# Performance work log

Hardware: AMD Instinct MI355X
Metric: run time of the kernel (lower is better)

The kernel has to match this reference:

```python
import jax, jax.numpy as jnp
import numpy as np

B, T, C, D = 8, 4096, 1024, 128  # batch, seq (=block_size), dim_embd, head_features

def setup_inputs() -> dict:
    key = jax.random.key(0)
    k1, k2, k3, k4 = jax.random.split(key, 4)
    s = 0.02
    return {
        "x": jax.random.normal(k1, (B, T, C), dtype=jnp.float32),
        "wq": jax.random.normal(k2, (C, D), dtype=jnp.float32) * s,
        "wk": jax.random.normal(k3, (C, D), dtype=jnp.float32) * s,
        "wv": jax.random.normal(k4, (C, D), dtype=jnp.float32) * s,
    }

def reference(x, wq, wk, wv):
    # q,k,v: [B,T,D]
    q = jnp.einsum('btc,cd->btd', x, wq)
    k = jnp.einsum('btc,cd->btd', x, wk)
    v = jnp.einsum('btc,cd->btd', x, wv)
    scale = k.shape[-1] ** -0.5
    wei = jnp.einsum('bqd,bkd->bqk', q, k) * scale  # [B,T,T]
    causal = jnp.tril(jnp.ones((T, T), dtype=bool))
    wei = jnp.where(causal, wei, -jnp.inf)
    attn = jax.nn.softmax(wei, axis=-1)  # dropout p=0.0 -> identity
    out = jnp.einsum('bqk,bkd->bqd', attn, v)  # [B,T,D]
    return out
```

## Files before the change

### kernel.cpp

```cpp
#include <hip/hip_runtime.h>

#define TT 4096
#define CC 1024
#define DD 128

typedef __attribute__((ext_vector_type(8))) short s16x8;
typedef __attribute__((ext_vector_type(4))) short s16x4;
typedef __attribute__((ext_vector_type(8))) __bf16 bf16x8;
typedef __attribute__((ext_vector_type(4))) float f32x4;

__device__ __forceinline__ short f2bf(float f) {
    union { float f; unsigned u; } v; v.f = f;
    unsigned r = v.u + 0x7fffu + ((v.u >> 16) & 1u);
    return (short)(r >> 16);
}

__device__ __forceinline__ unsigned cvt_pk(float lo, float hi) {
    unsigned r;
    asm("v_cvt_pk_bf16_f32 %0, %1, %2" : "=v"(r) : "v"(lo), "v"(hi));
    return r;
}

__device__ __forceinline__ f32x4 mfma16(s16x8 a, s16x8 b, f32x4 c) {
    return __builtin_amdgcn_mfma_f32_16x16x32_bf16(
        __builtin_bit_cast(bf16x8, a), __builtin_bit_cast(bf16x8, b), c, 0, 0, 0);
}

__device__ __forceinline__ void gload_lds16(const short* g, short* l) {
    __builtin_amdgcn_global_load_lds(
        (const __attribute__((address_space(1))) void*)g,
        (__attribute__((address_space(3))) void*)l, 16, 0, 0);
}

__global__ void wt_kernel(const float* __restrict__ wq, const float* __restrict__ wk,
                          const float* __restrict__ wv, short* __restrict__ wT) {
    int idx = blockIdx.x * 256 + threadIdx.x;
    int d = idx & 127;
    int c = (idx >> 7) & 1023;
    int wsel = idx >> 17;
    const float* w = (wsel == 0) ? wq : (wsel == 1) ? wk : wv;
    float v = w[(size_t)c * DD + d];
    if (wsel == 0) v *= 0.08838834764831845f;
    wT[(size_t)wsel * DD * CC + (size_t)d * CC + c] = f2bf(v);
}

__global__ __launch_bounds__(512)
void qkv_kernel(const float* __restrict__ x, const short* __restrict__ wT,
                short* __restrict__ qo, short* __restrict__ ko, short* __restrict__ vTo) {
    __shared__ short lw[2][384 * 64];
    const int mt = blockIdx.x;
    const int tid = threadIdx.x, lane = tid & 63, wid = tid >> 6;
    const int l15 = lane & 15, g = lane >> 4;
    const int wm = wid >> 1, wn = wid & 1;
    const int arow = mt * 128 + wm * 32 + l15;
    const float* xr0 = x + (size_t)arow * CC + g * 8;
    const float* xr1 = xr0 + (size_t)16 * CC;

    const f32x4 fz = {0.f, 0.f, 0.f, 0.f};
    f32x4 acc[2][12];
#pragma unroll
    for (int mr = 0; mr < 2; mr++)
#pragma unroll
        for (int nr = 0; nr < 12; nr++) acc[mr][nr] = fz;

    const int swr = wid * 48;
    const short* wsrc = wT + (size_t)(swr + (lane >> 3)) * CC + (lane & 7) * 8;

    float4 pa[2][2][2];
#define LOADA(kc) do { \
    _Pragma("unroll") for (int mr_ = 0; mr_ < 2; mr_++) \
    _Pragma("unroll") for (int ks_ = 0; ks_ < 2; ks_++) { \
        const float* p_ = (mr_ ? xr1 : xr0) + (kc) * 64 + ks_ * 32; \
        pa[mr_][ks_][0] = *(const float4*)p_; \
        pa[mr_][ks_][1] = *(const float4*)(p_ + 4); } \
} while (0)
#define STAGEW(kc, buf) do { \
    _Pragma("unroll") for (int j_ = 0; j_ < 6; j_++) \
        gload_lds16(wsrc + (size_t)(j_ * 8) * CC + (kc) * 64, &lw[buf][(swr + j_ * 8) * 64]); \
} while (0)

    LOADA(0);
    STAGEW(0, 0);
    asm volatile("s_waitcnt vmcnt(0)" ::: "memory");
    __builtin_amdgcn_s_barrier();
    int cur = 0;

    for (int kc = 0; kc < 16; kc++) {
        s16x8 af[2][2];
#pragma unroll
        for (int mr = 0; mr < 2; mr++)
#pragma unroll
            for (int ks = 0; ks < 2; ks++) {
                union { unsigned u[4]; s16x8 v; } cv;
                cv.u[0] = cvt_pk(pa[mr][ks][0].x, pa[mr][ks][0].y);
                cv.u[1] = cvt_pk(pa[mr][ks][0].z, pa[mr][ks][0].w);
                cv.u[2] = cvt_pk(pa[mr][ks][1].x, pa[mr][ks][1].y);
                cv.u[3] = cvt_pk(pa[mr][ks][1].z, pa[mr][ks][1].w);
                af[mr][ks] = cv.v;
            }
        if (kc < 15) { LOADA(kc + 1); STAGEW(kc + 1, cur ^ 1); }
        __builtin_amdgcn_s_setprio(1);
#pragma unroll
        for (int ks = 0; ks < 2; ks++)
#pragma unroll
            for (int nr = 0; nr < 12; nr++) {
                const s16x8 bfg = *(const s16x8*)
                    &lw[cur][(wn * 192 + nr * 16 + l15) * 64 + ks * 32 + g * 8];
                acc[0][nr] = mfma16(af[0][ks], bfg, acc[0][nr]);
                acc[1][nr] = mfma16(af[1][ks], bfg, acc[1][nr]);
            }
        __builtin_amdgcn_s_setprio(0);
        asm volatile("s_waitcnt vmcnt(0) lgkmcnt(0)" ::: "memory");
        __builtin_amdgcn_s_barrier();
        cur ^= 1;
    }

    const int bidx = mt >> 5;
    const int tb = (mt & 31) * 128 + wm * 32;
#pragma unroll
    for (int mr = 0; mr < 2; mr++)
#pragma unroll
        for (int nr = 0; nr < 12; nr++) {
            const int n = wn * 192 + nr * 16 + l15;
            if (n < 256) {
                short* dst; int d;
                if (n < 128) { dst = qo; d = n; } else { dst = ko; d = n - 128; }
#pragma unroll
                for (int i = 0; i < 4; i++) {
                    int t = tb + mr * 16 + g * 4 + i;
                    dst[((size_t)bidx * TT + t) * DD + d] = f2bf(acc[mr][nr][i]);
                }
            } else {
                const int d = n - 256;
                const int t = tb + mr * 16 + g * 4;
                uint2 u;
                u.x = cvt_pk(acc[mr][nr][0], acc[mr][nr][1]);
                u.y = cvt_pk(acc[mr][nr][2], acc[mr][nr][3]);
                *(uint2*)(vTo + ((size_t)bidx * DD + d) * TT + t) = u;
            }
        }
}

__device__ __forceinline__ void attn_stage(const short* kT, const short* vT, int kv0,
                                           short* lkb, short* lvb, int wid, int lane) {
#pragma unroll
    for (int j = 0; j < 4; j++) {
        int rbk = wid * 16 + j * 4;
        int rk = rbk + (lane >> 4);
        int ck = (lane & 15) ^ (rk & 7);
        gload_lds16(kT + (size_t)(kv0 + rk) * DD + ck * 8, lkb + rbk * 128);
        int rbv = wid * 32 + j * 8;
        int dv = rbv + (lane >> 3);
        int cv = (lane & 7) ^ (dv & 7);
        gload_lds16(vT + (size_t)dv * TT + kv0 + cv * 8, lvb + rbv * 64);
    }
}

__global__ __launch_bounds__(256)
void attn_kernel(const short* __restrict__ qb, const short* __restrict__ kb,
                 const short* __restrict__ vb, float* __restrict__ out) {
    __shared__ short lk[2][64 * 128];
    __shared__ short lv[2][128 * 64];
    __shared__ short lp[4 * 16 * 64];
    const int qt = 63 - blockIdx.x;
    const int b = blockIdx.y;
    const int tid = threadIdx.x, lane = tid & 63, wid = tid >> 6;
    const int l15 = lane & 15, g = lane >> 4;
    const int wq0 = qt * 64 + wid * 16;

    s16x8 qf[4];
    {
        const short* qp = qb + ((size_t)b * TT + wq0 + l15) * DD + g * 8;
#pragma unroll
        for (int ks = 0; ks < 4; ks++) qf[ks] = *(const s16x8*)(qp + ks * 32);
    }
    const f32x4 fz = {0.f, 0.f, 0.f, 0.f};
    f32x4 o[8];
#pragma unroll
    for (int n = 0; n < 8; n++) o[n] = fz;
    float rmax = -1e30f, rsum = 0.f;

    const short* kT = kb + (size_t)b * TT * DD;
    const short* vT = vb + (size_t)b * DD * TT;

    attn_stage(kT, vT, 0, lk[0], lv[0], wid, lane);
    asm volatile("s_waitcnt vmcnt(0)" ::: "memory");
    __builtin_amdgcn_s_barrier();
    int cur = 0;

    for (int kvt = 0; kvt <= qt; kvt++) {
        if (kvt < qt) attn_stage(kT, vT, (kvt + 1) * 64, lk[cur ^ 1], lv[cur ^ 1], wid, lane);
        const int kv0 = kvt * 64;
        const char* lkc = (const char*)&lk[cur][0];
        const char* lvc = (const char*)&lv[cur][0];

        f32x4 s[4];
        __builtin_amdgcn_s_setprio(1);
#pragma unroll
        for (int sub = 0; sub < 4; sub++) {
            f32x4 a = fz;
#pragma unroll
            for (int ks = 0; ks < 4; ks++) {
                int row = sub * 16 + l15;
                int byte = (row * 256 + ks * 64 + g * 16) ^ ((row & 7) << 4);
                s16x8 kf = *(const s16x8*)(lkc + byte);
                a = mfma16(kf, qf[ks], a);
            }
            s[sub] = a;
        }
        __builtin_amdgcn_s_setprio(0);
        if (kvt == qt) {
#pragma unroll
            for (int sub = 0; sub < 4; sub++)
#pragma unroll
                for (int i = 0; i < 4; i++) {
                    int k = kv0 + sub * 16 + 4 * g + i;
                    if (k > wq0 + l15) s[sub][i] = -1e30f;
                }
        }
        float m0 = s[0][0];
#pragma unroll
        for (int sub = 0; sub < 4; sub++)
#pragma unroll
            for (int i = 0; i < 4; i++) m0 = fmaxf(m0, s[sub][i]);
        m0 = fmaxf(m0, __shfl_xor(m0, 16));
        m0 = fmaxf(m0, __shfl_xor(m0, 32));
        float mnew = fmaxf(rmax, m0);
        float scal = __expf(rmax - mnew);
        rmax = mnew;
        float ls = 0.f;
#pragma unroll
        for (int sub = 0; sub < 4; sub++)
#pragma unroll
            for (int i = 0; i < 4; i++) {
                float p = __expf(s[sub][i] - mnew);
                s[sub][i] = p;
                ls += p;
            }
        ls += __shfl_xor(ls, 16);
        ls += __shfl_xor(ls, 32);
        rsum = rsum * scal + ls;
#pragma unroll
        for (int sub = 0; sub < 4; sub++) {
            uint2 w01;
            w01.x = cvt_pk(s[sub][0], s[sub][1]);
            w01.y = cvt_pk(s[sub][2], s[sub][3]);
            int byte = (l15 * 128 + sub * 32 + g * 8) ^ ((l15 & 7) << 4);
            *(uint2*)((char*)lp + wid * 2048 + byte) = w01;
        }
#pragma unroll
        for (int n = 0; n < 8; n++)
#pragma unroll
            for (int i = 0; i < 4; i++) o[n][i] *= scal;
        __builtin_amdgcn_s_setprio(1);
#pragma unroll
        for (int ks2 = 0; ks2 < 2; ks2++) {
            int pbyte = (l15 * 128 + ks2 * 64 + g * 16) ^ ((l15 & 7) << 4);
            s16x8 pf = *(const s16x8*)((const char*)lp + wid * 2048 + pbyte);
#pragma unroll
            for (int n = 0; n < 8; n++) {
                int vrow = n * 16 + l15;
                int vbyte = (vrow * 128 + ks2 * 64 + g * 16) ^ ((vrow & 7) << 4);
                s16x8 vf = *(const s16x8*)(lvc + vbyte);
                o[n] = mfma16(vf, pf, o[n]);
            }
        }
        __builtin_amdgcn_s_setprio(0);
        asm volatile("s_waitcnt vmcnt(0) lgkmcnt(0)" ::: "memory");
        __builtin_amdgcn_s_barrier();
        cur ^= 1;
    }
    float inv = 1.0f / rsum;
    float* orow = out + ((size_t)b * TT + wq0 + l15) * DD;
#pragma unroll
    for (int n = 0; n < 8; n++) {
        float4 r;
        r.x = o[n][0] * inv; r.y = o[n][1] * inv;
        r.z = o[n][2] * inv; r.w = o[n][3] * inv;
        *(float4*)(orow + n * 16 + 4 * g) = r;
    }
}

extern "C" void kernel_launch(void* const* d_in, const int* in_sizes, int n_in,
                              void* d_out, int out_size, void* d_ws, size_t ws_size,
                              hipStream_t stream) {
    const float* x  = (const float*)d_in[0];
    const float* wq = (const float*)d_in[1];
    const float* wk = (const float*)d_in[2];
    const float* wv = (const float*)d_in[3];
    float* out = (float*)d_out;
    char* ws = (char*)d_ws;
    short* wT = (short*)ws;
    short* qb = (short*)(ws + 786432);
    short* kb = (short*)(ws + 786432 + 8388608);
    short* vb = (short*)(ws + 786432 + 16777216);

    wt_kernel<<<1536, 256, 0, stream>>>(wq, wk, wv, wT);
    qkv_kernel<<<256, 512, 0, stream>>>(x, wT, qb, kb, vb);
    attn_kernel<<<dim3(64, 8), 256, 0, stream>>>(qb, kb, vb, out);
}
```

Baseline: 181.5 us.

## Pair short and long causal query tiles in one 8-wave attention block

Each attention block now holds 8 waves: four handle query tile p and four handle tile 63-p, so every block does about the same causal work and the grid shrinks to 256 blocks. The K/V tiles loaded into shared memory are shared by both query tiles, cutting redundant global loads. The cost is that waves on the short tile sit idle at the barrier for the rest of the loop, and the block needs more shared memory and more threads.

```diff
diff --git a/kernel.cpp b/kernel.cpp
--- a/kernel.cpp
+++ b/kernel.cpp
@@ -141,32 +141,35 @@
         }
 }
 
-__device__ __forceinline__ void attn_stage(const short* kT, const short* vT, int kv0,
-                                           short* lkb, short* lvb, int wid, int lane) {
-#pragma unroll
-    for (int j = 0; j < 4; j++) {
-        int rbk = wid * 16 + j * 4;
+__device__ __forceinline__ void attn_stage8(const short* kT, const short* vT, int kv0,
+                                            short* lkb, short* lvb, int wid, int lane) {
+#pragma unroll
+    for (int j = 0; j < 2; j++) {
+        int rbk = wid * 8 + j * 4;
         int rk = rbk + (lane >> 4);
         int ck = (lane & 15) ^ (rk & 7);
         gload_lds16(kT + (size_t)(kv0 + rk) * DD + ck * 8, lkb + rbk * 128);
-        int rbv = wid * 32 + j * 8;
+        int rbv = wid * 16 + j * 8;
         int dv = rbv + (lane >> 3);
         int cv = (lane & 7) ^ (dv & 7);
         gload_lds16(vT + (size_t)dv * TT + kv0 + cv * 8, lvb + rbv * 64);
     }
 }
 
-__global__ __launch_bounds__(256)
+__global__ __launch_bounds__(512)
 void attn_kernel(const short* __restrict__ qb, const short* __restrict__ kb,
                  const short* __restrict__ vb, float* __restrict__ out) {
     __shared__ short lk[2][64 * 128];
     __shared__ short lv[2][128 * 64];
-    __shared__ short lp[4 * 16 * 64];
-    const int qt = 63 - blockIdx.x;
-    const int b = blockIdx.y;
+    __shared__ short lp[8 * 16 * 64];
+    const int id = blockIdx.x;
+    const int b = id & 7;
+    const int p = id >> 3;
     const int tid = threadIdx.x, lane = tid & 63, wid = tid >> 6;
     const int l15 = lane & 15, g = lane >> 4;
-    const int wq0 = qt * 64 + wid * 16;
+    const int qt_w = (wid < 4) ? p : 63 - p;
+    const int wq0 = qt_w * 64 + (wid & 3) * 16;
+    const int tmax = 63 - p;
 
     s16x8 qf[4];
     {
@@ -183,89 +186,91 @@
     const short* kT = kb + (size_t)b * TT * DD;
     const short* vT = vb + (size_t)b * DD * TT;
 
-    attn_stage(kT, vT, 0, lk[0], lv[0], wid, lane);
+    attn_stage8(kT, vT, 0, lk[0], lv[0], wid, lane);
     asm volatile("s_waitcnt vmcnt(0)" ::: "memory");
     __builtin_amdgcn_s_barrier();
     int cur = 0;
 
-    for (int kvt = 0; kvt <= qt; kvt++) {
-        if (kvt < qt) attn_stage(kT, vT, (kvt + 1) * 64, lk[cur ^ 1], lv[cur ^ 1], wid, lane);
-        const int kv0 = kvt * 64;
-        const char* lkc = (const char*)&lk[cur][0];
-        const char* lvc = (const char*)&lv[cur][0];
-
-        f32x4 s[4];
-        __builtin_amdgcn_s_setprio(1);
-#pragma unroll
-        for (int sub = 0; sub < 4; sub++) {
-            f32x4 a = fz;
-#pragma unroll
-            for (int ks = 0; ks < 4; ks++) {
-                int row = sub * 16 + l15;
-                int byte = (row * 256 + ks * 64 + g * 16) ^ ((row & 7) << 4);
-                s16x8 kf = *(const s16x8*)(lkc + byte);
-                a = mfma16(kf, qf[ks], a);
-            }
-            s[sub] = a;
+    for (int t = 0; t <= tmax; t++) {
+        if (t < tmax) attn_stage8(kT, vT, (t + 1) * 64, lk[cur ^ 1], lv[cur ^ 1], wid, lane);
+        if (t <= qt_w) {
+            const int kv0 = t * 64;
+            const char* lkc = (const char*)&lk[cur][0];
+            const char* lvc = (const char*)&lv[cur][0];
+
+            f32x4 s[4];
+            __builtin_amdgcn_s_setprio(1);
+#pragma unroll
+            for (int sub = 0; sub < 4; sub++) {
+                f32x4 a = fz;
+#pragma unroll
+                for (int ks = 0; ks < 4; ks++) {
+                    int row = sub * 16 + l15;
+                    int byte = (row * 256 + ks * 64 + g * 16) ^ ((row & 7) << 4);
+                    s16x8 kf = *(const s16x8*)(lkc + byte);
+                    a = mfma16(kf, qf[ks], a);
+                }
+                s[sub] = a;
+            }
+            __builtin_amdgcn_s_setprio(0);
+            if (t == qt_w) {
+#pragma unroll
+                for (int sub = 0; sub < 4; sub++)
+#pragma unroll
+                    for (int i = 0; i < 4; i++) {
+                        int k = kv0 + sub * 16 + 4 * g + i;
+                        if (k > wq0 + l15) s[sub][i] = -1e30f;
+                    }
+            }
+            float m0 = s[0][0];
+#pragma unroll
+            for (int sub = 0; sub < 4; sub++)
+#pragma unroll
+                for (int i = 0; i < 4; i++) m0 = fmaxf(m0, s[sub][i]);
+            m0 = fmaxf(m0, __shfl_xor(m0, 16));
+            m0 = fmaxf(m0, __shfl_xor(m0, 32));
+            float mnew = fmaxf(rmax, m0);
+            float scal = __expf(rmax - mnew);
+            rmax = mnew;
+            float ls = 0.f;
+#pragma unroll
+            for (int sub = 0; sub < 4; sub++)
+#pragma unroll
+                for (int i = 0; i < 4; i++) {
+                    float pv = __expf(s[sub][i] - mnew);
+                    s[sub][i] = pv;
+                    ls += pv;
+                }
+            ls += __shfl_xor(ls, 16);
+            ls += __shfl_xor(ls, 32);
+            rsum = rsum * scal + ls;
+#pragma unroll
+            for (int sub = 0; sub < 4; sub++) {
+                uint2 w01;
+                w01.x = cvt_pk(s[sub][0], s[sub][1]);
+                w01.y = cvt_pk(s[sub][2], s[sub][3]);
+                int byte = (l15 * 128 + sub * 32 + g * 8) ^ ((l15 & 7) << 4);
+                *(uint2*)((char*)lp + wid * 2048 + byte) = w01;
+            }
+#pragma unroll
+            for (int n = 0; n < 8; n++)
+#pragma unroll
+                for (int i = 0; i < 4; i++) o[n][i] *= scal;
+            __builtin_amdgcn_s_setprio(1);
+#pragma unroll
+            for (int ks2 = 0; ks2 < 2; ks2++) {
+                int pbyte = (l15 * 128 + ks2 * 64 + g * 16) ^ ((l15 & 7) << 4);
+                s16x8 pf = *(const s16x8*)((const char*)lp + wid * 2048 + pbyte);
+#pragma unroll
+                for (int n = 0; n < 8; n++) {
+                    int vrow = n * 16 + l15;
+                    int vbyte = (vrow * 128 + ks2 * 64 + g * 16) ^ ((vrow & 7) << 4);
+                    s16x8 vf = *(const s16x8*)(lvc + vbyte);
+                    o[n] = mfma16(vf, pf, o[n]);
+                }
+            }
+            __builtin_amdgcn_s_setprio(0);
         }
-        __builtin_amdgcn_s_setprio(0);
-        if (kvt == qt) {
-#pragma unroll
-            for (int sub = 0; sub < 4; sub++)
-#pragma unroll
-                for (int i = 0; i < 4; i++) {
-                    int k = kv0 + sub * 16 + 4 * g + i;
-                    if (k > wq0 + l15) s[sub][i] = -1e30f;
-                }
-        }
-        float m0 = s[0][0];
-#pragma unroll
-        for (int sub = 0; sub < 4; sub++)
-#pragma unroll
-            for (int i = 0; i < 4; i++) m0 = fmaxf(m0, s[sub][i]);
-        m0 = fmaxf(m0, __shfl_xor(m0, 16));
-        m0 = fmaxf(m0, __shfl_xor(m0, 32));
-        float mnew = fmaxf(rmax, m0);
-        float scal = __expf(rmax - mnew);
-        rmax = mnew;
-        float ls = 0.f;
-#pragma unroll
-        for (int sub = 0; sub < 4; sub++)
-#pragma unroll
-            for (int i = 0; i < 4; i++) {
-                float p = __expf(s[sub][i] - mnew);
-                s[sub][i] = p;
-                ls += p;
-            }
-        ls += __shfl_xor(ls, 16);
-        ls += __shfl_xor(ls, 32);
-        rsum = rsum * scal + ls;
-#pragma unroll
-        for (int sub = 0; sub < 4; sub++) {
-            uint2 w01;
-            w01.x = cvt_pk(s[sub][0], s[sub][1]);
-            w01.y = cvt_pk(s[sub][2], s[sub][3]);
-            int byte = (l15 * 128 + sub * 32 + g * 8) ^ ((l15 & 7) << 4);
-            *(uint2*)((char*)lp + wid * 2048 + byte) = w01;
-        }
-#pragma unroll
-        for (int n = 0; n < 8; n++)
-#pragma unroll
-            for (int i = 0; i < 4; i++) o[n][i] *= scal;
-        __builtin_amdgcn_s_setprio(1);
-#pragma unroll
-        for (int ks2 = 0; ks2 < 2; ks2++) {
-            int pbyte = (l15 * 128 + ks2 * 64 + g * 16) ^ ((l15 & 7) << 4);
-            s16x8 pf = *(const s16x8*)((const char*)lp + wid * 2048 + pbyte);
-#pragma unroll
-            for (int n = 0; n < 8; n++) {
-                int vrow = n * 16 + l15;
-                int vbyte = (vrow * 128 + ks2 * 64 + g * 16) ^ ((vrow & 7) << 4);
-                s16x8 vf = *(const s16x8*)(lvc + vbyte);
-                o[n] = mfma16(vf, pf, o[n]);
-            }
-        }
-        __builtin_amdgcn_s_setprio(0);
         asm volatile("s_waitcnt vmcnt(0) lgkmcnt(0)" ::: "memory");
         __builtin_amdgcn_s_barrier();
         cur ^= 1;
@@ -297,5 +302,5 @@
 
     wt_kernel<<<1536, 256, 0, stream>>>(wq, wk, wv, wT);
     qkv_kernel<<<256, 512, 0, stream>>>(x, wT, qb, kb, vb);
-    attn_kernel<<<dim3(64, 8), 256, 0, stream>>>(qb, kb, vb, out);
-}
+    attn_kernel<<<256, 512, 0, stream>>>(qb, kb, vb, out);
+}
```

Result: faster. 168.3 us (-7.3%).

## Split KV range into chunks of 16 tiles with a separate combine kernel

Applied to the files above, without the earlier changes.

The attention kernel now splits each query tile's causal KV range into chunks of up to 16 tiles across a new grid dimension, flash-decoding style. Chunks write unnormalized partial outputs plus per-row max and sum to workspace, and a new combine kernel merges them with log-sum-exp rescaling. The aim is to even out the causal load imbalance, where late query tiles did up to 64 iterations, and to raise the block count from 512 for better CU occupancy. The cost is about 50 MB of extra fp32 partial traffic, many empty early-exit blocks, and an extra kernel launch.

```diff
diff --git a/kernel.cpp b/kernel.cpp
--- a/kernel.cpp
+++ b/kernel.cpp
@@ -158,15 +158,26 @@
 
 __global__ __launch_bounds__(256)
 void attn_kernel(const short* __restrict__ qb, const short* __restrict__ kb,
-                 const short* __restrict__ vb, float* __restrict__ out) {
+                 const short* __restrict__ vb, float* __restrict__ out,
+                 float* __restrict__ opart, float2* __restrict__ mlpart) {
+    const int qt = blockIdx.x;
+    const int c  = blockIdx.y;
+    const int b  = blockIdx.z;
+    const int t0 = c * 16;
+    if (t0 > qt) return;
+    const int t1 = (t0 + 16 < qt + 1) ? t0 + 16 : qt + 1;
+    const int nc = (qt >> 4) + 1;
+
     __shared__ short lk[2][64 * 128];
     __shared__ short lv[2][128 * 64];
-    __shared__ short lp[4 * 16 * 64];
-    const int qt = 63 - blockIdx.x;
-    const int b = blockIdx.y;
+    __shared__ short lp[4][1024];
     const int tid = threadIdx.x, lane = tid & 63, wid = tid >> 6;
     const int l15 = lane & 15, g = lane >> 4;
     const int wq0 = qt * 64 + wid * 16;
+    const short* kT = kb + (size_t)b * TT * DD;
+    const short* vT = vb + (size_t)b * DD * TT;
+    char* lpw = (char*)&lp[wid][0];
+    const f32x4 fz = {0.f, 0.f, 0.f, 0.f};
 
     s16x8 qf[4];
     {
@@ -174,23 +185,19 @@
 #pragma unroll
         for (int ks = 0; ks < 4; ks++) qf[ks] = *(const s16x8*)(qp + ks * 32);
     }
-    const f32x4 fz = {0.f, 0.f, 0.f, 0.f};
     f32x4 o[8];
 #pragma unroll
     for (int n = 0; n < 8; n++) o[n] = fz;
     float rmax = -1e30f, rsum = 0.f;
 
-    const short* kT = kb + (size_t)b * TT * DD;
-    const short* vT = vb + (size_t)b * DD * TT;
-
-    attn_stage(kT, vT, 0, lk[0], lv[0], wid, lane);
+    attn_stage(kT, vT, t0 * 64, lk[0], lv[0], wid, lane);
     asm volatile("s_waitcnt vmcnt(0)" ::: "memory");
     __builtin_amdgcn_s_barrier();
     int cur = 0;
 
-    for (int kvt = 0; kvt <= qt; kvt++) {
-        if (kvt < qt) attn_stage(kT, vT, (kvt + 1) * 64, lk[cur ^ 1], lv[cur ^ 1], wid, lane);
-        const int kv0 = kvt * 64;
+    for (int t = t0; t < t1; t++) {
+        if (t + 1 < t1) attn_stage(kT, vT, (t + 1) * 64, lk[cur ^ 1], lv[cur ^ 1], wid, lane);
+        const int kv0 = t * 64;
         const char* lkc = (const char*)&lk[cur][0];
         const char* lvc = (const char*)&lv[cur][0];
 
@@ -209,7 +216,7 @@
             s[sub] = a;
         }
         __builtin_amdgcn_s_setprio(0);
-        if (kvt == qt) {
+        if (t == qt) {
 #pragma unroll
             for (int sub = 0; sub < 4; sub++)
 #pragma unroll
@@ -233,9 +240,9 @@
         for (int sub = 0; sub < 4; sub++)
 #pragma unroll
             for (int i = 0; i < 4; i++) {
-                float p = __expf(s[sub][i] - mnew);
-                s[sub][i] = p;
-                ls += p;
+                float pv = __expf(s[sub][i] - mnew);
+                s[sub][i] = pv;
+                ls += pv;
             }
         ls += __shfl_xor(ls, 16);
         ls += __shfl_xor(ls, 32);
@@ -246,7 +253,7 @@
             w01.x = cvt_pk(s[sub][0], s[sub][1]);
             w01.y = cvt_pk(s[sub][2], s[sub][3]);
             int byte = (l15 * 128 + sub * 32 + g * 8) ^ ((l15 & 7) << 4);
-            *(uint2*)((char*)lp + wid * 2048 + byte) = w01;
+            *(uint2*)(lpw + byte) = w01;
         }
 #pragma unroll
         for (int n = 0; n < 8; n++)
@@ -256,7 +263,7 @@
 #pragma unroll
         for (int ks2 = 0; ks2 < 2; ks2++) {
             int pbyte = (l15 * 128 + ks2 * 64 + g * 16) ^ ((l15 & 7) << 4);
-            s16x8 pf = *(const s16x8*)((const char*)lp + wid * 2048 + pbyte);
+            s16x8 pf = *(const s16x8*)(lpw + pbyte);
 #pragma unroll
             for (int n = 0; n < 8; n++) {
                 int vrow = n * 16 + l15;
@@ -270,14 +277,75 @@
         __builtin_amdgcn_s_barrier();
         cur ^= 1;
     }
-    float inv = 1.0f / rsum;
-    float* orow = out + ((size_t)b * TT + wq0 + l15) * DD;
-#pragma unroll
-    for (int n = 0; n < 8; n++) {
-        float4 r;
-        r.x = o[n][0] * inv; r.y = o[n][1] * inv;
-        r.z = o[n][2] * inv; r.w = o[n][3] * inv;
-        *(float4*)(orow + n * 16 + 4 * g) = r;
+
+    const int r = wid * 16 + l15;
+    if (nc == 1) {
+        float inv = 1.0f / rsum;
+        float* orow = out + ((size_t)b * TT + qt * 64 + r) * DD;
+#pragma unroll
+        for (int n = 0; n < 8; n++) {
+            float4 w;
+            w.x = o[n][0] * inv; w.y = o[n][1] * inv;
+            w.z = o[n][2] * inv; w.w = o[n][3] * inv;
+            *(float4*)(orow + n * 16 + 4 * g) = w;
+        }
+    } else {
+        const size_t pb = ((size_t)b * 48 + (qt - 16)) * 4 + c;
+        float* prow = opart + pb * (64 * 128) + (size_t)r * 128;
+#pragma unroll
+        for (int n = 0; n < 8; n++) {
+            float4 w;
+            w.x = o[n][0]; w.y = o[n][1]; w.z = o[n][2]; w.w = o[n][3];
+            *(float4*)(prow + n * 16 + 4 * g) = w;
+        }
+        if (g == 0) {
+            float2 s2; s2.x = rmax; s2.y = rsum;
+            mlpart[pb * 64 + r] = s2;
+        }
+    }
+}
+
+__global__ __launch_bounds__(256)
+void comb_kernel(const float* __restrict__ opart, const float2* __restrict__ mlpart,
+                 float* __restrict__ out) {
+    const int qtm = blockIdx.x;
+    const int b = blockIdx.y;
+    const int qt = 16 + qtm;
+    const int nc = (qt >> 4) + 1;
+    const int tid = threadIdx.x;
+    const int row = tid >> 2, quad = tid & 3;
+    const size_t base = ((size_t)b * 48 + qtm) * 4;
+
+    float M = -3e38f;
+    for (int cc = 0; cc < nc; cc++)
+        M = fmaxf(M, mlpart[(base + cc) * 64 + row].x);
+
+    float acc[32];
+#pragma unroll
+    for (int k = 0; k < 32; k++) acc[k] = 0.f;
+    float L = 0.f;
+    for (int cc = 0; cc < nc; cc++) {
+        float2 s = mlpart[(base + cc) * 64 + row];
+        float wgt = __expf(s.x - M);
+        L += wgt * s.y;
+        const float* src = opart + (base + cc) * (64 * 128) + (size_t)row * 128 + quad * 32;
+#pragma unroll
+        for (int k = 0; k < 8; k++) {
+            float4 v = *(const float4*)(src + k * 4);
+            acc[k * 4 + 0] += wgt * v.x;
+            acc[k * 4 + 1] += wgt * v.y;
+            acc[k * 4 + 2] += wgt * v.z;
+            acc[k * 4 + 3] += wgt * v.w;
+        }
+    }
+    float inv = 1.0f / L;
+    float* dst = out + ((size_t)b * TT + qt * 64 + row) * DD + quad * 32;
+#pragma unroll
+    for (int k = 0; k < 8; k++) {
+        float4 w;
+        w.x = acc[k * 4 + 0] * inv; w.y = acc[k * 4 + 1] * inv;
+        w.z = acc[k * 4 + 2] * inv; w.w = acc[k * 4 + 3] * inv;
+        *(float4*)(dst + k * 4) = w;
     }
 }
 
@@ -294,8 +362,11 @@
     short* qb = (short*)(ws + 786432);
     short* kb = (short*)(ws + 786432 + 8388608);
     short* vb = (short*)(ws + 786432 + 16777216);
+    float* opart = (float*)(ws + 786432 + 25165824);
+    float2* mlpart = (float2*)(ws + 786432 + 25165824 + 50331648);
 
     wt_kernel<<<1536, 256, 0, stream>>>(wq, wk, wv, wT);
     qkv_kernel<<<256, 512, 0, stream>>>(x, wT, qb, kb, vb);
-    attn_kernel<<<dim3(64, 8), 256, 0, stream>>>(qb, kb, vb, out);
-}
+    attn_kernel<<<dim3(64, 4, 8), 256, 0, stream>>>(qb, kb, vb, out, opart, mlpart);
+    comb_kernel<<<dim3(48, 8), 256, 0, stream>>>(opart, mlpart, out);
+}
```

New measurement: 170.7 us. 6.0% less time.
